# Kernel tuning notes

Measured on AMD Instinct MI355X. Metric: run time of the kernel, lower is better.

The kernel has to match this reference:

```python
import jax, jax.numpy as jnp
import numpy as np

N = 8192
F_IN = 256
F_OUT = 64
ALPHA = 0.2  # leaky-relu negative slope
NEG_INF = -9e15


def setup_inputs() -> dict:
    key = jax.random.key(0)
    k1, k2, k3, k4 = jax.random.split(key, 4)
    h = jax.random.normal(k1, (N, F_IN), dtype=jnp.float32)
    adj = jax.random.randint(k2, (N, N), 0, 2, dtype=jnp.int32)
    W = jax.random.normal(k3, (F_IN, F_OUT), dtype=jnp.float32)
    a = jax.random.normal(k4, (2 * F_OUT, 1), dtype=jnp.float32)
    return {"h": h, "adj": adj, "W": W, "a": a}


def reference(h, adj, W, a):
    # Wh: [N, F_OUT]
    Wh = h @ W
    # Decompose a = [a1; a2]: e_ij = leakyrelu(a1^T Wh_i + a2^T Wh_j),
    # identical math to concat([Wh_i, Wh_j]) @ a without the O(N^2*2F) tensor.
    a1 = a[:F_OUT, 0]
    a2 = a[F_OUT:, 0]
    s1 = Wh @ a1  # [N]
    s2 = Wh @ a2  # [N]
    e = s1[:, None] + s2[None, :]  # [N, N]
    e = jnp.where(e > 0, e, ALPHA * e)  # leaky relu
    scores = jnp.where(adj > 0, e, NEG_INF)
    attention = jax.nn.softmax(scores, axis=1)  # [N, N]
    h_prime = attention @ Wh  # [N, F_OUT]
    return h_prime
```

## Files before the change

kernel.cpp:

```cpp
#include <hip/hip_runtime.h>

#define N 8192
#define F_IN 256
#define F_OUT 64
#define ALPHA 0.2f
#define LOG2E 1.4426950408889634f

typedef __attribute__((ext_vector_type(8))) short bf16x8;
typedef __attribute__((ext_vector_type(4))) float f32x4;
typedef __attribute__((ext_vector_type(4))) int i32x4;
typedef __attribute__((ext_vector_type(4))) unsigned u32x4;
typedef __attribute__((ext_vector_type(4))) unsigned short u16x4;

__device__ __forceinline__ unsigned short f2bf(float x) {
    unsigned u = __float_as_uint(x);
    u = (u + 0x7FFFu + ((u >> 16) & 1u)) >> 16;
    return (unsigned short)u;
}
__device__ __forceinline__ float bf2f(unsigned short h) {
    return __uint_as_float((unsigned)h << 16);
}
__device__ __forceinline__ float fast_exp2(float x) {
#if __has_builtin(__builtin_amdgcn_exp2f)
    return __builtin_amdgcn_exp2f(x);
#else
    return __expf(x * 0.6931471805599453f);
#endif
}

__device__ __forceinline__ void load2_bypass(const int* p0, const int* p1,
                                             i32x4& r0, i32x4& r1) {
    asm volatile(
        "global_load_dwordx4 %0, %2, off sc0 sc1 nt\n\t"
        "global_load_dwordx4 %1, %3, off sc0 sc1 nt\n\t"
        "s_waitcnt vmcnt(0)"
        : "=&v"(r0), "=&v"(r1)
        : "v"(p0), "v"(p1)
        : "memory");
}

__global__ __launch_bounds__(256) void prep_kernel(
    const float* __restrict__ W, const float* __restrict__ a,
    float* __restrict__ Wa1, float* __restrict__ Wa2,
    unsigned short* __restrict__ WbTh, unsigned short* __restrict__ WbTl) {
    __shared__ float Wl[F_IN][F_OUT + 1];
    __shared__ float al[2 * F_OUT];
    const int t = threadIdx.x;
    for (int it = 0; it < 16; ++it) {
        const int idx = it * 1024 + t * 4;
        const f32x4 v = *(const f32x4*)&W[idx];
        const int r = idx >> 6, c = idx & 63;
        Wl[r][c] = v[0]; Wl[r][c + 1] = v[1]; Wl[r][c + 2] = v[2]; Wl[r][c + 3] = v[3];
    }
    if (t < 128) al[t] = a[t];
    __syncthreads();
    float x1 = 0.f, x2 = 0.f;
#pragma unroll 8
    for (int f = 0; f < F_OUT; ++f) {
        const float wv = Wl[t][f];
        x1 += wv * al[f];
        x2 += wv * al[F_OUT + f];
    }
    Wa1[t] = x1; Wa2[t] = x2;
    const int f = t >> 2, k0 = (t & 3) * 64;
    for (int kk = 0; kk < 64; kk += 8) {
        u32x4 ph, pl;
#pragma unroll
        for (int u = 0; u < 4; ++u) {
            const float w0 = Wl[k0 + kk + 2 * u][f];
            const float w1 = Wl[k0 + kk + 2 * u + 1][f];
            const unsigned short h0 = f2bf(w0), h1 = f2bf(w1);
            const unsigned short l0 = f2bf(w0 - bf2f(h0)), l1 = f2bf(w1 - bf2f(h1));
            ph[u] = (unsigned)h0 | ((unsigned)h1 << 16);
            pl[u] = (unsigned)l0 | ((unsigned)l1 << 16);
        }
        *(u32x4*)&WbTh[f * F_IN + k0 + kk] = ph;
        *(u32x4*)&WbTl[f * F_IN + k0 + kk] = pl;
    }
}

__global__ __launch_bounds__(256) void score_kernel(
    const float* __restrict__ h, const float* __restrict__ Wa1,
    const float* __restrict__ Wa2, float* __restrict__ s1c, float* __restrict__ s2c) {
    __shared__ float w1l[F_IN], w2l[F_IN];
    const int t = threadIdx.x, wave = t >> 6, lane = t & 63;
    w1l[t] = Wa1[t]; w2l[t] = Wa2[t];
    __syncthreads();
    const int row0 = blockIdx.x * 16 + wave * 4;
    const f32x4 wa1 = *(const f32x4*)&w1l[lane * 4];
    const f32x4 wa2 = *(const f32x4*)&w2l[lane * 4];
#pragma unroll
    for (int r = 0; r < 4; ++r) {
        const f32x4 hv = *(const f32x4*)(h + (size_t)(row0 + r) * F_IN + lane * 4);
        float d1 = hv[0] * wa1[0] + hv[1] * wa1[1] + hv[2] * wa1[2] + hv[3] * wa1[3];
        float d2 = hv[0] * wa2[0] + hv[1] * wa2[1] + hv[2] * wa2[2] + hv[3] * wa2[3];
#pragma unroll
        for (int off = 32; off; off >>= 1) {
            d1 += __shfl_down(d1, off, 64);
            d2 += __shfl_down(d2, off, 64);
        }
        if (lane == 0) { s1c[row0 + r] = d1 * LOG2E; s2c[row0 + r] = d2 * LOG2E; }
    }
}

__global__ __launch_bounds__(256) void whT_kernel(
    const float* __restrict__ h, const unsigned short* __restrict__ WbTh,
    const unsigned short* __restrict__ WbTl, unsigned short* __restrict__ WhT) {
    const int t = threadIdx.x;
    const int nt = t >> 6, lane = t & 63;
    const int mq = lane & 15, quad = lane >> 4;
    const int i0 = blockIdx.x * 16;
    const float* hp = h + (size_t)(i0 + mq) * F_IN + quad * 8;
    const unsigned short* bph = WbTh + (nt * 16 + mq) * F_IN + quad * 8;
    const unsigned short* bpl = WbTl + (nt * 16 + mq) * F_IN + quad * 8;
    f32x4 acc = {0.f, 0.f, 0.f, 0.f};
#pragma unroll
    for (int kk = 0; kk < 8; ++kk) {
        const f32x4 h0 = *(const f32x4*)(hp + kk * 32);
        const f32x4 h1 = *(const f32x4*)(hp + kk * 32 + 4);
        bf16x8 ah, al;
#pragma unroll
        for (int u = 0; u < 8; ++u) {
            const float v = (u < 4) ? h0[u] : h1[u - 4];
            const unsigned short hi = f2bf(v);
            ah[u] = (short)hi;
            al[u] = (short)f2bf(v - bf2f(hi));
        }
        const bf16x8 bh = *(const bf16x8*)(bph + kk * 32);
        const bf16x8 bl = *(const bf16x8*)(bpl + kk * 32);
        acc = __builtin_amdgcn_mfma_f32_16x16x32_bf16(ah, bh, acc, 0, 0, 0);
        acc = __builtin_amdgcn_mfma_f32_16x16x32_bf16(al, bh, acc, 0, 0, 0);
        acc = __builtin_amdgcn_mfma_f32_16x16x32_bf16(ah, bl, acc, 0, 0, 0);
    }
    u16x4 o;
#pragma unroll
    for (int r = 0; r < 4; ++r) o[r] = f2bf(acc[r]);
    *(u16x4*)&WhT[(size_t)(nt * 16 + mq) * N + i0 + quad * 4] = o;
}

__global__ __launch_bounds__(256) void compress_kernel(
    const int* __restrict__ adj, const float* __restrict__ s2c,
    const float* __restrict__ s1c,
    unsigned char* __restrict__ maskbits, float* __restrict__ mrowc) {
    __shared__ float red[4];
    const int t = threadIdx.x, wave = t >> 6, lane = t & 63;
    const int row = blockIdx.x;
    const int odd = t & 1;
    const int* __restrict__ arow = adj + (size_t)row * N;
    float mx = -3.0e38f;

#pragma unroll
    for (int pp = 0; pp < 4; ++pp) {
        const int i40 = (2 * pp) * 256 + t;
        const int i41 = (2 * pp + 1) * 256 + t;
        i32x4 a0, a1;
        load2_bypass(arow + i40 * 4, arow + i41 * 4, a0, a1);
        const f32x4 s0 = *(const f32x4*)(s2c + i40 * 4);
        const f32x4 s1 = *(const f32x4*)(s2c + i41 * 4);

        const unsigned nib0 =
            (a0[0] > 0 ? 1u : 0u) | (a0[1] > 0 ? 2u : 0u) |
            (a0[2] > 0 ? 4u : 0u) | (a0[3] > 0 ? 8u : 0u);
        const unsigned nib1 =
            (a1[0] > 0 ? 1u : 0u) | (a1[1] > 0 ? 2u : 0u) |
            (a1[2] > 0 ? 4u : 0u) | (a1[3] > 0 ? 8u : 0u);
#pragma unroll
        for (int u = 0; u < 4; ++u) {
            mx = fmaxf(mx, (a0[u] > 0) ? s0[u] : -3.0e38f);
            mx = fmaxf(mx, (a1[u] > 0) ? s1[u] : -3.0e38f);
        }
        const unsigned pn0 = (unsigned)__shfl_xor((int)nib0, 1, 64);
        const unsigned pn1 = (unsigned)__shfl_xor((int)nib1, 1, 64);
        if (!odd) {
            maskbits[(size_t)row * (N / 8) + (i40 >> 1)] = (unsigned char)(nib0 | (pn0 << 4));
            maskbits[(size_t)row * (N / 8) + (i41 >> 1)] = (unsigned char)(nib1 | (pn1 << 4));
        }
    }
#pragma unroll
    for (int off = 32; off; off >>= 1) mx = fmaxf(mx, __shfl_down(mx, off, 64));
    if (lane == 0) red[wave] = mx;
    __syncthreads();
    if (t == 0) {
        const float mm = fmaxf(fmaxf(red[0], red[1]), fmaxf(red[2], red[3]));
        const float xm = s1c[row] + mm;
        mrowc[row] = fmaxf(xm, ALPHA * xm);
    }
}

#define AROWS 16
__global__ __launch_bounds__(512, 8) void attn_kernel(
    const unsigned char* __restrict__ maskbits,
    const unsigned short* __restrict__ WhT,
    const float* __restrict__ s1c, const float* __restrict__ s2c,
    const float* __restrict__ mrowc, float* __restrict__ out) {
    __shared__ float s1l[AROWS], ml[AROWS];
    __shared__ __align__(16) float accbuf[8][AROWS][F_OUT];
    __shared__ float rowsums[8][AROWS];

    const int t = threadIdx.x, wave = t >> 6, lane = t & 63;
    const int i0 = blockIdx.x * AROWS;
    if (t < AROWS) { s1l[t] = s1c[i0 + t]; ml[t] = mrowc[i0 + t]; }
    __syncthreads();

    const int mq = lane & 15, quad = lane >> 4;
    const float s1m = s1l[mq];
    const float mr = ml[mq];
    const int jb0 = wave * 1024;

    const unsigned char* __restrict__ mbp =
        maskbits + (size_t)(i0 + mq) * (N / 8) + (jb0 >> 3) + quad;
    const float* __restrict__ sp = s2c + jb0 + quad * 8;
    const unsigned short* __restrict__ wp = WhT + (size_t)mq * N + jb0 + quad * 8;

    f32x4 acc0 = {0.f, 0.f, 0.f, 0.f}, acc1 = acc0, acc2 = acc0, acc3 = acc0, accS = acc0;
    bf16x8 onesf;
#pragma unroll
    for (int u = 0; u < 8; ++u) onesf[u] = (mq == 0) ? (short)0x3F80 : (short)0;

    for (int c = 0; c < 32; ++c) {
        const unsigned mbyte = mbp[c * 4];
        const f32x4 v0 = *(const f32x4*)(sp + c * 32);
        const f32x4 v1 = *(const f32x4*)(sp + c * 32 + 4);
        const unsigned short* wpc = wp + c * 32;
        const bf16x8 b0 = *(const bf16x8*)(wpc);
        const bf16x8 b1 = *(const bf16x8*)(wpc + 16 * N);
        const bf16x8 b2 = *(const bf16x8*)(wpc + 32 * N);
        const bf16x8 b3 = *(const bf16x8*)(wpc + 48 * N);

        bf16x8 af;
#pragma unroll
        for (int jj = 0; jj < 8; ++jj) {
            const float s2k = (jj < 4) ? v0[jj] : v1[jj - 4];
            const float x = s1m + s2k;
            const float e = fmaxf(x, ALPHA * x);
            const float w = ((mbyte >> jj) & 1u) ? fast_exp2(e - mr) : 0.f;
            af[jj] = (short)(__float_as_uint(w) >> 16);
        }
        acc0 = __builtin_amdgcn_mfma_f32_16x16x32_bf16(af, b0, acc0, 0, 0, 0);
        acc1 = __builtin_amdgcn_mfma_f32_16x16x32_bf16(af, b1, acc1, 0, 0, 0);
        acc2 = __builtin_amdgcn_mfma_f32_16x16x32_bf16(af, b2, acc2, 0, 0, 0);
        acc3 = __builtin_amdgcn_mfma_f32_16x16x32_bf16(af, b3, acc3, 0, 0, 0);
        accS = __builtin_amdgcn_mfma_f32_16x16x32_bf16(af, onesf, accS, 0, 0, 0);
    }

#pragma unroll
    for (int r = 0; r < 4; ++r) {
        const int row = quad * 4 + r;
        accbuf[wave][row][0 + mq]  = acc0[r];
        accbuf[wave][row][16 + mq] = acc1[r];
        accbuf[wave][row][32 + mq] = acc2[r];
        accbuf[wave][row][48 + mq] = acc3[r];
        if (mq == 0) rowsums[wave][row] = accS[r];
    }
    __syncthreads();

    {
        const int row = t >> 5, f0 = (t & 31) * 2;
        float o0 = 0.f, o1 = 0.f, rs = 0.f;
#pragma unroll
        for (int w = 0; w < 8; ++w) {
            o0 += accbuf[w][row][f0];
            o1 += accbuf[w][row][f0 + 1];
            rs += rowsums[w][row];
        }
        const float inv = (rs > 0.f) ? 1.f / rs : 0.f;
        float2 st = {o0 * inv, o1 * inv};
        *(float2*)&out[(size_t)(i0 + row) * F_OUT + f0] = st;
    }
}

extern "C" void kernel_launch(void* const* d_in, const int* in_sizes, int n_in,
                              void* d_out, int out_size, void* d_ws, size_t ws_size,
                              hipStream_t stream) {
    const float* h   = (const float*)d_in[0];
    const int*   adj = (const int*)d_in[1];
    const float* W   = (const float*)d_in[2];
    const float* a   = (const float*)d_in[3];
    float* out = (float*)d_out;

    char* ws = (char*)d_ws;
    unsigned char* maskbits = (unsigned char*)ws;
    unsigned short* WhT = (unsigned short*)(ws + (size_t)N * (N / 8));
    float* s1c  = (float*)((char*)WhT + (size_t)F_OUT * N * 2);
    float* s2c  = s1c + N;
    float* mrowc = s2c + N;
    float* Wa1 = mrowc + N;
    float* Wa2 = Wa1 + F_IN;
    unsigned short* WbTh = (unsigned short*)(Wa2 + F_IN);
    unsigned short* WbTl = WbTh + F_OUT * F_IN;

    prep_kernel<<<1, 256, 0, stream>>>(W, a, Wa1, Wa2, WbTh, WbTl);
    score_kernel<<<N / 16, 256, 0, stream>>>(h, Wa1, Wa2, s1c, s2c);
    whT_kernel<<<N / 16, 256, 0, stream>>>(h, WbTh, WbTl, WhT);
    compress_kernel<<<N, 256, 0, stream>>>(adj, s2c, s1c, maskbits, mrowc);
    attn_kernel<<<N / AROWS, 512, 0, stream>>>(maskbits, WhT, s1c, s2c, mrowc, out);
}
```

Measured before the change: 446.8 us.

## Fuse adjacency compression into attention kernel with online softmax

Removes the separate compress pass that packed adj into bitmasks and precomputed row maxima. The attention kernel now reads the int32 adjacency directly with nontemporal loads prefetched one chunk ahead, and uses a flash-style running max with accumulator rescaling. Per-wave partial results are merged with exp-weighted correction. This saves one full pass over the 256MB adj and a kernel launch. In exchange it adds per-iteration shuffles, rescale multiplies and register pressure, and lowers the occupancy hint from 8 to 4.

```diff
diff --git a/kernel.cpp b/kernel.cpp
--- a/kernel.cpp
+++ b/kernel.cpp
@@ -5,6 +5,8 @@
 #define F_OUT 64
 #define ALPHA 0.2f
 #define LOG2E 1.4426950408889634f
+#define NEGBIG -3.0e38f
+#define MINIT -1.0e30f
 
 typedef __attribute__((ext_vector_type(8))) short bf16x8;
 typedef __attribute__((ext_vector_type(4))) float f32x4;
@@ -27,16 +29,8 @@
     return __expf(x * 0.6931471805599453f);
 #endif
 }
-
-__device__ __forceinline__ void load2_bypass(const int* p0, const int* p1,
-                                             i32x4& r0, i32x4& r1) {
-    asm volatile(
-        "global_load_dwordx4 %0, %2, off sc0 sc1 nt\n\t"
-        "global_load_dwordx4 %1, %3, off sc0 sc1 nt\n\t"
-        "s_waitcnt vmcnt(0)"
-        : "=&v"(r0), "=&v"(r1)
-        : "v"(p0), "v"(p1)
-        : "memory");
+__device__ __forceinline__ i32x4 ntload4(const int* p) {
+    return __builtin_nontemporal_load((const i32x4*)p);
 }
 
 __global__ __launch_bounds__(256) void prep_kernel(
@@ -138,77 +132,27 @@
     *(u16x4*)&WhT[(size_t)(nt * 16 + mq) * N + i0 + quad * 4] = o;
 }
 
-__global__ __launch_bounds__(256) void compress_kernel(
-    const int* __restrict__ adj, const float* __restrict__ s2c,
-    const float* __restrict__ s1c,
-    unsigned char* __restrict__ maskbits, float* __restrict__ mrowc) {
-    __shared__ float red[4];
-    const int t = threadIdx.x, wave = t >> 6, lane = t & 63;
-    const int row = blockIdx.x;
-    const int odd = t & 1;
-    const int* __restrict__ arow = adj + (size_t)row * N;
-    float mx = -3.0e38f;
-
-#pragma unroll
-    for (int pp = 0; pp < 4; ++pp) {
-        const int i40 = (2 * pp) * 256 + t;
-        const int i41 = (2 * pp + 1) * 256 + t;
-        i32x4 a0, a1;
-        load2_bypass(arow + i40 * 4, arow + i41 * 4, a0, a1);
-        const f32x4 s0 = *(const f32x4*)(s2c + i40 * 4);
-        const f32x4 s1 = *(const f32x4*)(s2c + i41 * 4);
-
-        const unsigned nib0 =
-            (a0[0] > 0 ? 1u : 0u) | (a0[1] > 0 ? 2u : 0u) |
-            (a0[2] > 0 ? 4u : 0u) | (a0[3] > 0 ? 8u : 0u);
-        const unsigned nib1 =
-            (a1[0] > 0 ? 1u : 0u) | (a1[1] > 0 ? 2u : 0u) |
-            (a1[2] > 0 ? 4u : 0u) | (a1[3] > 0 ? 8u : 0u);
-#pragma unroll
-        for (int u = 0; u < 4; ++u) {
-            mx = fmaxf(mx, (a0[u] > 0) ? s0[u] : -3.0e38f);
-            mx = fmaxf(mx, (a1[u] > 0) ? s1[u] : -3.0e38f);
-        }
-        const unsigned pn0 = (unsigned)__shfl_xor((int)nib0, 1, 64);
-        const unsigned pn1 = (unsigned)__shfl_xor((int)nib1, 1, 64);
-        if (!odd) {
-            maskbits[(size_t)row * (N / 8) + (i40 >> 1)] = (unsigned char)(nib0 | (pn0 << 4));
-            maskbits[(size_t)row * (N / 8) + (i41 >> 1)] = (unsigned char)(nib1 | (pn1 << 4));
-        }
-    }
-#pragma unroll
-    for (int off = 32; off; off >>= 1) mx = fmaxf(mx, __shfl_down(mx, off, 64));
-    if (lane == 0) red[wave] = mx;
-    __syncthreads();
-    if (t == 0) {
-        const float mm = fmaxf(fmaxf(red[0], red[1]), fmaxf(red[2], red[3]));
-        const float xm = s1c[row] + mm;
-        mrowc[row] = fmaxf(xm, ALPHA * xm);
-    }
-}
-
 #define AROWS 16
-__global__ __launch_bounds__(512, 8) void attn_kernel(
-    const unsigned char* __restrict__ maskbits,
+__global__ __launch_bounds__(512, 4) void attn_kernel(
+    const int* __restrict__ adj,
     const unsigned short* __restrict__ WhT,
     const float* __restrict__ s1c, const float* __restrict__ s2c,
-    const float* __restrict__ mrowc, float* __restrict__ out) {
-    __shared__ float s1l[AROWS], ml[AROWS];
+    float* __restrict__ out) {
+    __shared__ float s1l[AROWS];
     __shared__ __align__(16) float accbuf[8][AROWS][F_OUT];
     __shared__ float rowsums[8][AROWS];
+    __shared__ float rowmaxs[8][AROWS];
 
     const int t = threadIdx.x, wave = t >> 6, lane = t & 63;
     const int i0 = blockIdx.x * AROWS;
-    if (t < AROWS) { s1l[t] = s1c[i0 + t]; ml[t] = mrowc[i0 + t]; }
+    if (t < AROWS) s1l[t] = s1c[i0 + t];
     __syncthreads();
 
     const int mq = lane & 15, quad = lane >> 4;
     const float s1m = s1l[mq];
-    const float mr = ml[mq];
     const int jb0 = wave * 1024;
 
-    const unsigned char* __restrict__ mbp =
-        maskbits + (size_t)(i0 + mq) * (N / 8) + (jb0 >> 3) + quad;
+    const int* __restrict__ ap = adj + (size_t)(i0 + mq) * N + jb0 + quad * 8;
     const float* __restrict__ sp = s2c + jb0 + quad * 8;
     const unsigned short* __restrict__ wp = WhT + (size_t)mq * N + jb0 + quad * 8;
 
@@ -217,8 +161,17 @@
 #pragma unroll
     for (int u = 0; u < 8; ++u) onesf[u] = (mq == 0) ? (short)0x3F80 : (short)0;
 
+    float m = MINIT;
+    i32x4 a0 = ntload4(ap);
+    i32x4 a1 = ntload4(ap + 4);
+
+#pragma unroll 2
     for (int c = 0; c < 32; ++c) {
-        const unsigned mbyte = mbp[c * 4];
+        i32x4 na0 = a0, na1 = a1;
+        if (c + 1 < 32) {
+            na0 = ntload4(ap + (c + 1) * 32);
+            na1 = ntload4(ap + (c + 1) * 32 + 4);
+        }
         const f32x4 v0 = *(const f32x4*)(sp + c * 32);
         const f32x4 v1 = *(const f32x4*)(sp + c * 32 + 4);
         const unsigned short* wpc = wp + c * 32;
@@ -227,13 +180,36 @@
         const bf16x8 b2 = *(const bf16x8*)(wpc + 32 * N);
         const bf16x8 b3 = *(const bf16x8*)(wpc + 48 * N);
 
-        bf16x8 af;
+        float es[8];
+        float tm = NEGBIG;
 #pragma unroll
         for (int jj = 0; jj < 8; ++jj) {
             const float s2k = (jj < 4) ? v0[jj] : v1[jj - 4];
             const float x = s1m + s2k;
             const float e = fmaxf(x, ALPHA * x);
-            const float w = ((mbyte >> jj) & 1u) ? fast_exp2(e - mr) : 0.f;
+            const int av = (jj < 4) ? a0[jj] : a1[jj - 4];
+            const float sel = (av > 0) ? e : NEGBIG;
+            es[jj] = sel;
+            tm = fmaxf(tm, sel);
+        }
+        tm = fmaxf(tm, __shfl_xor(tm, 16, 64));
+        tm = fmaxf(tm, __shfl_xor(tm, 32, 64));
+        const float nm = fmaxf(m, tm);
+        const float f = fast_exp2(m - nm);
+        m = nm;
+        float fr0 = __shfl(f, quad * 4 + 0, 64);
+        float fr1 = __shfl(f, quad * 4 + 1, 64);
+        float fr2 = __shfl(f, quad * 4 + 2, 64);
+        float fr3 = __shfl(f, quad * 4 + 3, 64);
+        acc0[0] *= fr0; acc1[0] *= fr0; acc2[0] *= fr0; acc3[0] *= fr0; accS[0] *= fr0;
+        acc0[1] *= fr1; acc1[1] *= fr1; acc2[1] *= fr1; acc3[1] *= fr1; accS[1] *= fr1;
+        acc0[2] *= fr2; acc1[2] *= fr2; acc2[2] *= fr2; acc3[2] *= fr2; accS[2] *= fr2;
+        acc0[3] *= fr3; acc1[3] *= fr3; acc2[3] *= fr3; acc3[3] *= fr3; accS[3] *= fr3;
+
+        bf16x8 af;
+#pragma unroll
+        for (int jj = 0; jj < 8; ++jj) {
+            const float w = fast_exp2(es[jj] - m);
             af[jj] = (short)(__float_as_uint(w) >> 16);
         }
         acc0 = __builtin_amdgcn_mfma_f32_16x16x32_bf16(af, b0, acc0, 0, 0, 0);
@@ -241,6 +217,7 @@
         acc2 = __builtin_amdgcn_mfma_f32_16x16x32_bf16(af, b2, acc2, 0, 0, 0);
         acc3 = __builtin_amdgcn_mfma_f32_16x16x32_bf16(af, b3, acc3, 0, 0, 0);
         accS = __builtin_amdgcn_mfma_f32_16x16x32_bf16(af, onesf, accS, 0, 0, 0);
+        a0 = na0; a1 = na1;
     }
 
 #pragma unroll
@@ -252,16 +229,21 @@
         accbuf[wave][row][48 + mq] = acc3[r];
         if (mq == 0) rowsums[wave][row] = accS[r];
     }
+    if (lane < AROWS) rowmaxs[wave][lane] = m;
     __syncthreads();
 
     {
         const int row = t >> 5, f0 = (t & 31) * 2;
+        float M = rowmaxs[0][row];
+#pragma unroll
+        for (int w = 1; w < 8; ++w) M = fmaxf(M, rowmaxs[w][row]);
         float o0 = 0.f, o1 = 0.f, rs = 0.f;
 #pragma unroll
         for (int w = 0; w < 8; ++w) {
-            o0 += accbuf[w][row][f0];
-            o1 += accbuf[w][row][f0 + 1];
-            rs += rowsums[w][row];
+            const float fw = fast_exp2(rowmaxs[w][row] - M);
+            o0 += accbuf[w][row][f0] * fw;
+            o1 += accbuf[w][row][f0 + 1] * fw;
+            rs += rowsums[w][row] * fw;
         }
         const float inv = (rs > 0.f) ? 1.f / rs : 0.f;
         float2 st = {o0 * inv, o1 * inv};
@@ -279,19 +261,16 @@
     float* out = (float*)d_out;
 
     char* ws = (char*)d_ws;
-    unsigned char* maskbits = (unsigned char*)ws;
-    unsigned short* WhT = (unsigned short*)(ws + (size_t)N * (N / 8));
-    float* s1c  = (float*)((char*)WhT + (size_t)F_OUT * N * 2);
+    unsigned short* WhT = (unsigned short*)ws;
+    float* s1c  = (float*)(ws + (size_t)F_OUT * N * 2);
     float* s2c  = s1c + N;
-    float* mrowc = s2c + N;
-    float* Wa1 = mrowc + N;
-    float* Wa2 = Wa1 + F_IN;
+    float* Wa1  = s2c + N;
+    float* Wa2  = Wa1 + F_IN;
     unsigned short* WbTh = (unsigned short*)(Wa2 + F_IN);
     unsigned short* WbTl = WbTh + F_OUT * F_IN;
 
     prep_kernel<<<1, 256, 0, stream>>>(W, a, Wa1, Wa2, WbTh, WbTl);
     score_kernel<<<N / 16, 256, 0, stream>>>(h, Wa1, Wa2, s1c, s2c);
     whT_kernel<<<N / 16, 256, 0, stream>>>(h, WbTh, WbTl, WhT);
-    compress_kernel<<<N, 256, 0, stream>>>(adj, s2c, s1c, maskbits, mrowc);
-    attn_kernel<<<N / AROWS, 512, 0, stream>>>(maskbits, WhT, s1c, s2c, mrowc, out);
-}
+    attn_kernel<<<N / AROWS, 512, 0, stream>>>(adj, WhT, s1c, s2c, out);
+}
```

Measured after the change: 440.8 us. No clear change (-1.3%).
